# Kernel tuning notes

Measured on AMD Instinct MI355X. Metric: run time of the kernel, lower is better.

Reference implementation:

```python
import jax, jax.numpy as jnp
import numpy as np
from jax import lax

# dims: T timesteps, CIN=6 DoG channels, HxW image; F conv filters, K kernel
T, CIN, H, W_IN = 15, 6, 512, 512
F, K, PAD = 64, 5, 2
THRESH = 15.0
K_WTA, RADIUS = 5, 2  # self.k1, self.r1


def setup_inputs() -> dict:
    key = jax.random.key(0)
    k1, k2 = jax.random.split(key)
    # cumulative binary spike wave: once a unit spikes it stays 1 (SpykeTorch convention)
    ev = (jax.random.uniform(k1, (T, CIN, H, W_IN)) < 0.02).astype(jnp.float32)
    x = jnp.clip(jnp.cumsum(ev, axis=0), 0.0, 1.0)
    w = 0.8 + 0.05 * jax.random.normal(k2, (F, CIN, K, K), dtype=jnp.float32)
    return {"x": x, "w": w}


def _pool_pad(x, pad):
    # sf.pooling(x, 2, 2): max-pool 2x2 stride 2; sf.pad: zero pad
    x = lax.reduce_window(x, -jnp.inf, lax.max, (1, 1, 2, 2), (1, 1, 2, 2), 'VALID')
    return jnp.pad(x, ((0, 0), (0, 0), (pad, pad), (pad, pad)))


def _fire(pot, thr):
    # sf.fire(pot, thr, True): zero sub-threshold potentials, spikes = sign
    tp = jnp.where(pot < thr, 0.0, pot)
    return jnp.sign(tp), tp


def _pointwise_inhibition(pot):
    # keep, per spatial site, only the feature with the earliest (then strongest) spike
    T_ = pot.shape[0]
    max_vals = jnp.max(pot, axis=1, keepdims=True)      # [T,1,H,W]
    max_idx = jnp.argmax(pot, axis=1, keepdims=True)    # [T,1,H,W]
    clamp = jnp.sign(max_vals)                          # 1 where any feature active
    earliest = jnp.clip(T_ - jnp.sum(clamp, axis=0, keepdims=True), 0, T_ - 1).astype(jnp.int32)  # [1,1,H,W]
    winners = jnp.take_along_axis(max_idx, earliest, axis=0)  # [1,1,H,W] winning feature
    has_spike = clamp[-1:]                              # [1,1,H,W] any spike by last step
    ch = jnp.arange(pot.shape[1]).reshape(1, -1, 1, 1)
    coef = jnp.where(ch == winners, has_spike, 0.0)     # scatter of winner coeff
    return pot * coef


def _get_k_winners(pot, spikes, k, radius):
    # NMS-like radius-based k-winners-take-all over [F,H,W]
    T_ = pot.shape[0]
    earliest = jnp.clip(T_ - jnp.sum(spikes, axis=0, keepdims=True), 0, T_ - 1).astype(jnp.int32)
    values = jnp.take_along_axis(pot, earliest, axis=0)  # potential at earliest spike
    trunc = spikes * values
    v = jnp.max(trunc) * T_  # large bias favoring earlier spikes
    total = jnp.sum(trunc + spikes * v, axis=0)          # [F,H,W]
    Fc, Hh, Ww = total.shape
    feat = jnp.arange(Fc).reshape(-1, 1, 1)
    row = jnp.arange(Hh).reshape(1, -1, 1)
    col = jnp.arange(Ww).reshape(1, 1, -1)
    winners = []
    for _ in range(k):  # small fixed k (5), fine to unroll
        idx = jnp.argmax(total)
        val = jnp.reshape(total, (-1,))[idx]
        f, r, c = jnp.unravel_index(idx, total.shape)
        active = val != 0
        win = jnp.where(active, jnp.stack([f, r, c]).astype(jnp.int32),
                        jnp.full((3,), -1, jnp.int32))
        winners.append(win)
        suppress = (feat == f) | ((jnp.abs(row - r) <= radius) & (jnp.abs(col - c) <= radius))
        total = jnp.where(active & suppress, 0.0, total)
    return jnp.stack(winners)  # [k,3] with -1 rows when fewer winners exist


def reference(x, w):
    inp = _pool_pad(x, PAD)  # [T,6,260,260]
    pot = lax.conv_general_dilated(inp, w, (1, 1), 'VALID',
                                   dimension_numbers=('NCHW', 'OIHW', 'NCHW'))  # [T,F,256,256]
    spk, pot = _fire(pot, THRESH)
    pot = _pointwise_inhibition(pot)
    spk = jnp.sign(pot)
    winners = _get_k_winners(pot, spk, K_WTA, RADIUS)
    return spk, winners
```

## Files before the change

### kernel.cpp

```cpp
#include <hip/hip_runtime.h>
#include <hip/hip_bf16.h>

#define T_ 15
#define CIN_ 6
#define F_ 64
#define HW_ 256
#define PW_ 260
#define THRESH_ 15.0f
#define TAU_NEVER 15


__global__ __launch_bounds__(256) void pool_tau(const float* __restrict__ x,
                                                unsigned char* __restrict__ tau) {
    int idx = blockIdx.x * 256 + threadIdx.x;
    if (idx >= CIN_ * HW_ * HW_) return;
    int xx = idx & 255;
    int yy = (idx >> 8) & 255;
    int c  = idx >> 16;
    const float* base = x + ((size_t)c * 512 + 2 * yy) * 512 + 2 * xx;
    int tval = TAU_NEVER;
    for (int t = 0; t < T_; ++t) {
        float2 a = *(const float2*)(base);
        float2 b = *(const float2*)(base + 512);
        if (a.x > 0.f || a.y > 0.f || b.x > 0.f || b.y > 0.f) { tval = t; break; }
        base += (size_t)CIN_ * 512 * 512;
    }
    tau[(c * PW_ + (yy + 2)) * PW_ + (xx + 2)] = (unsigned char)tval;
}

__global__ __launch_bounds__(256, 2) void phaseA(const unsigned char* __restrict__ tau,
                                                 const float* __restrict__ w,
                                                 int* __restrict__ rec_wch,
                                                 float* __restrict__ rec_val,
                                                 int* __restrict__ rec_e,
                                                 unsigned int* __restrict__ gmaxp) {
    __shared__ float wl[F_ * 172];
    __shared__ unsigned char tw[CIN_ * 144];
    __shared__ float red[64 * 65];
    __shared__ float pm[64 * 5];
    __shared__ int   pa[64 * 5];
    __shared__ unsigned char donef[64];
    __shared__ int doneG[4];
    __shared__ int doneAll;
    __shared__ int bmaxBits;

    const int tid = threadIdx.x;
    const int f = tid & 63;
    const int g = tid >> 6;
    const int gx = (g & 1) * 4;
    const int gy = (g >> 1) * 4;
    const int px0 = blockIdx.x * 8;
    const int py0 = blockIdx.y * 8;

    if (tid < 64) donef[tid] = 0;
    if (tid < 4) doneG[tid] = 0;
    if (tid == 0) { doneAll = 0; bmaxBits = 0; }

    for (int idx = tid; idx < F_ * 150; idx += 256) {
        int ff = idx / 150, r = idx - ff * 150;
        int c = r / 25, k = r - c * 25;
        wl[ff * 172 + c * 28 + k] = w[idx];
    }
    for (int idx = tid; idx < CIN_ * 144; idx += 256) {
        int c = idx / 144;
        int rem = idx - c * 144;
        int r = rem / 12;
        int xx = rem - r * 12;
        tw[idx] = tau[(c * PW_ + (py0 + r)) * PW_ + (px0 + xx)];
    }
    __syncthreads();

    for (int t = 0; t < T_; ++t) {
        bool waveActive = (doneG[g] < 16);

        if (waveActive) {
            float acc[16];
#pragma unroll
            for (int i = 0; i < 16; ++i) acc[i] = 0.0f;

            for (int c = 0; c < CIN_; ++c) {
                float win[8][8];
                const unsigned char* tb = &tw[c * 144 + gy * 12 + gx];
#pragma unroll
                for (int r = 0; r < 8; ++r) {
                    unsigned int lo = *(const unsigned int*)(tb + r * 12);
                    unsigned int hi = *(const unsigned int*)(tb + r * 12 + 4);
#pragma unroll
                    for (int b = 0; b < 4; ++b) {
                        win[r][b]     = (((lo >> (8 * b)) & 0xFF) <= (unsigned)t) ? 1.0f : 0.0f;
                        win[r][4 + b] = (((hi >> (8 * b)) & 0xFF) <= (unsigned)t) ? 1.0f : 0.0f;
                    }
                }
                float wr[28];
#pragma unroll
                for (int q = 0; q < 7; ++q)
                    *(float4*)&wr[4 * q] = *(const float4*)&wl[f * 172 + c * 28 + 4 * q];
#pragma unroll
                for (int ki = 0; ki < 5; ++ki)
#pragma unroll
                    for (int kj = 0; kj < 5; ++kj) {
                        float wv = wr[ki * 5 + kj];
#pragma unroll
                        for (int py = 0; py < 4; ++py)
#pragma unroll
                            for (int px = 0; px < 4; ++px)
                                acc[py * 4 + px] += win[py + ki][px + kj] * wv;
                    }
            }
#pragma unroll
            for (int i = 0; i < 16; ++i) {
                float v = acc[i];
                v = (v < THRESH_) ? 0.0f : v;
                int py = i >> 2, px = i & 3;
                int pxl = (gy + py) * 8 + (gx + px);
                red[pxl * 65 + f] = v;
            }
        }
        __syncthreads();

        {
            int pxl = tid & 63, ch = tid >> 6;
            if (!donef[pxl]) {
                float m = -1.0f; int a = 0;
#pragma unroll
                for (int k = 0; k < 16; ++k) {
                    float v = red[pxl * 65 + ch * 16 + k];
                    if (v > m) { m = v; a = ch * 16 + k; }
                }
                pm[pxl * 5 + ch] = m;
                pa[pxl * 5 + ch] = a;
            }
        }
        __syncthreads();

        if (tid < 64 && !donef[tid]) {
            float m = pm[tid * 5]; int a = pa[tid * 5];
#pragma unroll
            for (int ch = 1; ch < 4; ++ch) {
                float v = pm[tid * 5 + ch];
                if (v > m) { m = v; a = pa[tid * 5 + ch]; }
            }
            if (m > 0.0f) {
                int gyg = py0 + (tid >> 3), gxg = px0 + (tid & 7);
                int p = gyg * HW_ + gxg;
                rec_wch[p] = a;
                rec_val[p] = m;
                rec_e[p] = t;
                donef[tid] = 1;
                int gyp = tid >> 3, gxp = tid & 7;
                int gOf = ((gyp >= 4) ? 2 : 0) + ((gxp >= 4) ? 1 : 0);
                atomicAdd(&doneG[gOf], 1);
                atomicAdd(&doneAll, 1);
                atomicMax(&bmaxBits, __float_as_int(m));
            }
        }
        __syncthreads();
        if (doneAll == 64) break;
    }

    if (tid < 64 && !donef[tid]) {
        int gyg = py0 + (tid >> 3), gxg = px0 + (tid & 7);
        int p = gyg * HW_ + gxg;
        rec_wch[p] = -1;
        rec_val[p] = 0.0f;
        rec_e[p] = T_;
    }
    if (tid == 0 && bmaxBits != 0)
        atomicMax(gmaxp, (unsigned int)bmaxBits);
}

__global__ __launch_bounds__(256) void render(const int* __restrict__ rec_wch,
                                              const int* __restrict__ rec_e,
                                              float* __restrict__ out) {
    const int tid = threadIdx.x;
    const int t = blockIdx.y;
    const int px = blockIdx.x * 1024 + tid * 4;

    int4 wch4 = *(const int4*)(rec_wch + px);
    int4 e4   = *(const int4*)(rec_e + px);
    int s0 = (wch4.x >= 0 && t >= e4.x) ? wch4.x : -1;
    int s1 = (wch4.y >= 0 && t >= e4.y) ? wch4.y : -1;
    int s2 = (wch4.z >= 0 && t >= e4.z) ? wch4.z : -1;
    int s3 = (wch4.w >= 0 && t >= e4.w) ? wch4.w : -1;

    float* base = out + (((size_t)t * F_) << 16) + px;
#pragma unroll
    for (int f = 0; f < F_; ++f) {
        float4 v;
        v.x = (f == s0) ? 1.0f : 0.0f;
        v.y = (f == s1) ? 1.0f : 0.0f;
        v.z = (f == s2) ? 1.0f : 0.0f;
        v.w = (f == s3) ? 1.0f : 0.0f;
        *(float4*)(base + ((size_t)f << 16)) = v;
    }
}

__global__ __launch_bounds__(256) void compute_total(const int* __restrict__ rec_wch,
                                                     const float* __restrict__ rec_val,
                                                     const int* __restrict__ rec_e,
                                                     const unsigned int* __restrict__ gmaxp,
                                                     float* __restrict__ total) {
    int i = blockIdx.x * 256 + threadIdx.x;
    int wch = rec_wch[i];
    float g = __uint_as_float(*gmaxp);
    float v15 = 15.0f * g;
    float tot = 0.0f;
    if (wch >= 0) {
        int e = rec_e[i];
        float base = rec_val[i] + v15;
        for (int t = e; t < T_; ++t) tot += base;
    }
    total[i] = tot;
}

__global__ __launch_bounds__(256) void max_round(const float* __restrict__ total,
                                                 const int* __restrict__ rec_wch,
                                                 unsigned long long* __restrict__ slots,
                                                 int round) {
    __shared__ unsigned long long sred[256];
    int i = blockIdx.x * 256 + threadIdx.x;
    float v = total[i];
    unsigned long long key = 0ULL;
    if (v > 0.0f) {
        int fch = rec_wch[i];
        int r = i >> 8, c = i & 255;
        bool sup = false;
        for (int j = 0; j < round; ++j) {
            unsigned long long s = slots[j];
            if (s == 0ULL) continue;
            int fl = 0x7fffffff - (int)(unsigned int)(s & 0xffffffffu);
            int fj = fl >> 16, rj = (fl >> 8) & 255, cj = fl & 255;
            int dr = r - rj; if (dr < 0) dr = -dr;
            int dc = c - cj; if (dc < 0) dc = -dc;
            if (fch == fj || (dr <= 2 && dc <= 2)) sup = true;
        }
        if (!sup) {
            int fl = (fch << 16) | i;
            unsigned int comp = 0x7fffffffu - (unsigned int)fl;
            key = ((unsigned long long)__float_as_uint(v) << 32) | comp;
        }
    }
    sred[threadIdx.x] = key;
    __syncthreads();
    for (int s = 128; s > 0; s >>= 1) {
        if (threadIdx.x < s) {
            if (sred[threadIdx.x + s] > sred[threadIdx.x]) sred[threadIdx.x] = sred[threadIdx.x + s];
        }
        __syncthreads();
    }
    if (threadIdx.x == 0 && sred[0] != 0ULL)
        atomicMax(&slots[round], sred[0]);
}

__global__ void writer(const unsigned long long* __restrict__ slots,
                       float* __restrict__ out) {
    int r = threadIdx.x;
    if (r < 5) {
        unsigned long long s = slots[r];
        float* wout = out + (size_t)T_ * F_ * HW_ * HW_ + r * 3;
        if (s != 0ULL) {
            int fl = 0x7fffffff - (int)(unsigned int)(s & 0xffffffffu);
            wout[0] = (float)(fl >> 16);
            wout[1] = (float)((fl >> 8) & 255);
            wout[2] = (float)(fl & 255);
        } else {
            wout[0] = -1.0f; wout[1] = -1.0f; wout[2] = -1.0f;
        }
    }
}

extern "C" void kernel_launch(void* const* d_in, const int* in_sizes, int n_in,
                              void* d_out, int out_size, void* d_ws, size_t ws_size,
                              hipStream_t stream) {
    const float* x = (const float*)d_in[0];
    const float* w = (const float*)d_in[1];
    float* out = (float*)d_out;

    char* wsc = (char*)d_ws;
    unsigned char* tau = (unsigned char*)wsc;
    size_t off = (size_t)CIN_ * PW_ * PW_;
    int* rec_wch = (int*)(wsc + off);        off += 65536 * sizeof(int);
    float* rec_val = (float*)(wsc + off);    off += 65536 * sizeof(float);
    int* rec_e = (int*)(wsc + off);          off += 65536 * sizeof(int);
    float* total = (float*)(wsc + off);      off += 65536 * sizeof(float);
    unsigned long long* slots = (unsigned long long*)(wsc + off);  off += 5 * sizeof(unsigned long long);
    unsigned int* gmaxp = (unsigned int*)(wsc + off);

    hipMemsetAsync(tau, 0x0F, (size_t)CIN_ * PW_ * PW_, stream);
    hipMemsetAsync(slots, 0, 5 * sizeof(unsigned long long) + sizeof(unsigned int), stream);

    pool_tau<<<(CIN_ * HW_ * HW_ + 255) / 256, 256, 0, stream>>>(x, tau);
    phaseA<<<dim3(32, 32), 256, 0, stream>>>(tau, w, rec_wch, rec_val, rec_e, gmaxp);
    render<<<dim3(64, 15), 256, 0, stream>>>(rec_wch, rec_e, out);
    compute_total<<<256, 256, 0, stream>>>(rec_wch, rec_val, rec_e, gmaxp, total);
    for (int r = 0; r < 5; ++r)
        max_round<<<256, 256, 0, stream>>>(total, rec_wch, slots, r);
    writer<<<1, 64, 0, stream>>>(slots, out);
}
```

Measured before the change: 483.7 us.

## Replace shared-memory channel argmax with wave shuffles and binary-search first-spike time

New measurement: 471.3 us. 1.03x faster.

```diff
diff --git a/kernel.cpp b/kernel.cpp
--- a/kernel.cpp
+++ b/kernel.cpp
@@ -11,55 +11,64 @@
 
 
 __global__ __launch_bounds__(256) void pool_tau(const float* __restrict__ x,
-                                                unsigned char* __restrict__ tau) {
+                                                unsigned char* __restrict__ tau,
+                                                unsigned long long* __restrict__ slots,
+                                                unsigned int* __restrict__ gmaxp) {
     int idx = blockIdx.x * 256 + threadIdx.x;
-    if (idx >= CIN_ * HW_ * HW_) return;
-    int xx = idx & 255;
-    int yy = (idx >> 8) & 255;
-    int c  = idx >> 16;
-    const float* base = x + ((size_t)c * 512 + 2 * yy) * 512 + 2 * xx;
-    int tval = TAU_NEVER;
-    for (int t = 0; t < T_; ++t) {
-        float2 a = *(const float2*)(base);
-        float2 b = *(const float2*)(base + 512);
-        if (a.x > 0.f || a.y > 0.f || b.x > 0.f || b.y > 0.f) { tval = t; break; }
-        base += (size_t)CIN_ * 512 * 512;
-    }
-    tau[(c * PW_ + (yy + 2)) * PW_ + (xx + 2)] = (unsigned char)tval;
-}
-
-__global__ __launch_bounds__(256, 2) void phaseA(const unsigned char* __restrict__ tau,
+    if (idx < 5) slots[idx] = 0ULL;
+    if (idx == 5) *gmaxp = 0u;
+    if (idx >= CIN_ * PW_ * PW_) return;
+    int xx = idx % PW_;
+    int rest = idx / PW_;
+    int yy = rest % PW_;
+    int c = rest / PW_;
+    unsigned char tv = TAU_NEVER;
+    if (xx >= 2 && xx < 258 && yy >= 2 && yy < 258) {
+        int i = yy - 2, j = xx - 2;
+        const float* b0 = x + ((size_t)c * 512 + 2 * i) * 512 + 2 * j;
+        const size_t tstride = (size_t)CIN_ * 512 * 512;
+        {
+            const float* b = b0 + 14 * tstride;
+            float2 a = *(const float2*)b;
+            float2 d = *(const float2*)(b + 512);
+            if (a.x > 0.f || a.y > 0.f || d.x > 0.f || d.y > 0.f) {
+                int lo = 0, hi = 14;
+                while (lo < hi) {
+                    int mid = (lo + hi) >> 1;
+                    const float* bm = b0 + (size_t)mid * tstride;
+                    float2 am = *(const float2*)bm;
+                    float2 dm = *(const float2*)(bm + 512);
+                    bool on = (am.x > 0.f || am.y > 0.f || dm.x > 0.f || dm.y > 0.f);
+                    if (on) hi = mid; else lo = mid + 1;
+                }
+                tv = (unsigned char)lo;
+            }
+        }
+    }
+    tau[idx] = tv;
+}
+
+__global__ __launch_bounds__(256, 3) void phaseA(const unsigned char* __restrict__ tau,
                                                  const float* __restrict__ w,
                                                  int* __restrict__ rec_wch,
                                                  float* __restrict__ rec_val,
                                                  int* __restrict__ rec_e,
                                                  unsigned int* __restrict__ gmaxp) {
-    __shared__ float wl[F_ * 172];
+    __shared__ float wl2[150 * 64];
     __shared__ unsigned char tw[CIN_ * 144];
-    __shared__ float red[64 * 65];
-    __shared__ float pm[64 * 5];
-    __shared__ int   pa[64 * 5];
-    __shared__ unsigned char donef[64];
-    __shared__ int doneG[4];
-    __shared__ int doneAll;
-    __shared__ int bmaxBits;
+    __shared__ float wmax[4];
 
     const int tid = threadIdx.x;
-    const int f = tid & 63;
+    const int lane = tid & 63;
     const int g = tid >> 6;
     const int gx = (g & 1) * 4;
     const int gy = (g >> 1) * 4;
     const int px0 = blockIdx.x * 8;
     const int py0 = blockIdx.y * 8;
 
-    if (tid < 64) donef[tid] = 0;
-    if (tid < 4) doneG[tid] = 0;
-    if (tid == 0) { doneAll = 0; bmaxBits = 0; }
-
-    for (int idx = tid; idx < F_ * 150; idx += 256) {
-        int ff = idx / 150, r = idx - ff * 150;
-        int c = r / 25, k = r - c * 25;
-        wl[ff * 172 + c * 28 + k] = w[idx];
+    for (int idx = tid; idx < 9600; idx += 256) {
+        int k = idx >> 6, f = idx & 63;
+        wl2[idx] = w[f * 150 + k];
     }
     for (int idx = tid; idx < CIN_ * 144; idx += 256) {
         int c = idx / 144;
@@ -70,103 +79,78 @@
     }
     __syncthreads();
 
+    unsigned int done = 0;
+    int myw = -1, mye = T_;
+    float myv = 0.0f;
+    float wavemax = 0.0f;
+
     for (int t = 0; t < T_; ++t) {
-        bool waveActive = (doneG[g] < 16);
-
-        if (waveActive) {
-            float acc[16];
-#pragma unroll
-            for (int i = 0; i < 16; ++i) acc[i] = 0.0f;
-
-            for (int c = 0; c < CIN_; ++c) {
-                float win[8][8];
-                const unsigned char* tb = &tw[c * 144 + gy * 12 + gx];
-#pragma unroll
-                for (int r = 0; r < 8; ++r) {
-                    unsigned int lo = *(const unsigned int*)(tb + r * 12);
-                    unsigned int hi = *(const unsigned int*)(tb + r * 12 + 4);
-#pragma unroll
-                    for (int b = 0; b < 4; ++b) {
-                        win[r][b]     = (((lo >> (8 * b)) & 0xFF) <= (unsigned)t) ? 1.0f : 0.0f;
-                        win[r][4 + b] = (((hi >> (8 * b)) & 0xFF) <= (unsigned)t) ? 1.0f : 0.0f;
-                    }
-                }
-                float wr[28];
-#pragma unroll
-                for (int q = 0; q < 7; ++q)
-                    *(float4*)&wr[4 * q] = *(const float4*)&wl[f * 172 + c * 28 + 4 * q];
-#pragma unroll
-                for (int ki = 0; ki < 5; ++ki)
-#pragma unroll
-                    for (int kj = 0; kj < 5; ++kj) {
-                        float wv = wr[ki * 5 + kj];
-#pragma unroll
-                        for (int py = 0; py < 4; ++py)
-#pragma unroll
-                            for (int px = 0; px < 4; ++px)
-                                acc[py * 4 + px] += win[py + ki][px + kj] * wv;
-                    }
+        float acc[16];
+#pragma unroll
+        for (int i = 0; i < 16; ++i) acc[i] = 0.0f;
+
+        for (int c = 0; c < CIN_; ++c) {
+            float win[8][8];
+            const unsigned char* tb = &tw[c * 144 + gy * 12 + gx];
+#pragma unroll
+            for (int r = 0; r < 8; ++r) {
+                unsigned int lo = *(const unsigned int*)(tb + r * 12);
+                unsigned int hi = *(const unsigned int*)(tb + r * 12 + 4);
+#pragma unroll
+                for (int b = 0; b < 4; ++b) {
+                    win[r][b]     = (((lo >> (8 * b)) & 0xFF) <= (unsigned)t) ? 1.0f : 0.0f;
+                    win[r][4 + b] = (((hi >> (8 * b)) & 0xFF) <= (unsigned)t) ? 1.0f : 0.0f;
+                }
             }
 #pragma unroll
-            for (int i = 0; i < 16; ++i) {
-                float v = acc[i];
-                v = (v < THRESH_) ? 0.0f : v;
-                int py = i >> 2, px = i & 3;
-                int pxl = (gy + py) * 8 + (gx + px);
-                red[pxl * 65 + f] = v;
+            for (int ki = 0; ki < 5; ++ki)
+#pragma unroll
+                for (int kj = 0; kj < 5; ++kj) {
+                    float wv = wl2[((c * 25 + ki * 5 + kj) << 6) + lane];
+#pragma unroll
+                    for (int py = 0; py < 4; ++py)
+#pragma unroll
+                        for (int px = 0; px < 4; ++px)
+                            acc[py * 4 + px] += win[py + ki][px + kj] * wv;
+                }
+        }
+
+#pragma unroll
+        for (int i = 0; i < 16; ++i) {
+            if (done & (1u << i)) continue;
+            float v = acc[i];
+            v = (v < THRESH_) ? 0.0f : v;
+            if (__any(v > 0.0f)) {
+                unsigned long long key =
+                    ((unsigned long long)__float_as_uint(v) << 6) | (unsigned)(63 - lane);
+#pragma unroll
+                for (int m = 1; m < 64; m <<= 1) {
+                    unsigned long long o = __shfl_xor(key, m, 64);
+                    if (o > key) key = o;
+                }
+                float mv = __uint_as_float((unsigned int)(key >> 6));
+                int wf = 63 - (int)(key & 63ULL);
+                done |= (1u << i);
+                if (lane == i) { myw = wf; myv = mv; mye = t; }
+                wavemax = fmaxf(wavemax, mv);
             }
         }
-        __syncthreads();
-
-        {
-            int pxl = tid & 63, ch = tid >> 6;
-            if (!donef[pxl]) {
-                float m = -1.0f; int a = 0;
-#pragma unroll
-                for (int k = 0; k < 16; ++k) {
-                    float v = red[pxl * 65 + ch * 16 + k];
-                    if (v > m) { m = v; a = ch * 16 + k; }
-                }
-                pm[pxl * 5 + ch] = m;
-                pa[pxl * 5 + ch] = a;
-            }
-        }
-        __syncthreads();
-
-        if (tid < 64 && !donef[tid]) {
-            float m = pm[tid * 5]; int a = pa[tid * 5];
-#pragma unroll
-            for (int ch = 1; ch < 4; ++ch) {
-                float v = pm[tid * 5 + ch];
-                if (v > m) { m = v; a = pa[tid * 5 + ch]; }
-            }
-            if (m > 0.0f) {
-                int gyg = py0 + (tid >> 3), gxg = px0 + (tid & 7);
-                int p = gyg * HW_ + gxg;
-                rec_wch[p] = a;
-                rec_val[p] = m;
-                rec_e[p] = t;
-                donef[tid] = 1;
-                int gyp = tid >> 3, gxp = tid & 7;
-                int gOf = ((gyp >= 4) ? 2 : 0) + ((gxp >= 4) ? 1 : 0);
-                atomicAdd(&doneG[gOf], 1);
-                atomicAdd(&doneAll, 1);
-                atomicMax(&bmaxBits, __float_as_int(m));
-            }
-        }
-        __syncthreads();
-        if (doneAll == 64) break;
-    }
-
-    if (tid < 64 && !donef[tid]) {
-        int gyg = py0 + (tid >> 3), gxg = px0 + (tid & 7);
-        int p = gyg * HW_ + gxg;
-        rec_wch[p] = -1;
-        rec_val[p] = 0.0f;
-        rec_e[p] = T_;
-    }
-    if (tid == 0 && bmaxBits != 0)
-        atomicMax(gmaxp, (unsigned int)bmaxBits);
+        if (done == 0xFFFFu) break;
+    }
+
+    if (lane < 16) {
+        int py = lane >> 2, px = lane & 3;
+        int p = (py0 + gy + py) * HW_ + (px0 + gx + px);
+        rec_wch[p] = myw;
+        rec_val[p] = myv;
+        rec_e[p] = mye;
+    }
+    if (lane == 0) wmax[g] = wavemax;
+    __syncthreads();
+    if (tid == 0) {
+        float m = fmaxf(fmaxf(wmax[0], wmax[1]), fmaxf(wmax[2], wmax[3]));
+        if (m > 0.0f) atomicMax(gmaxp, __float_as_uint(m));
+    }
 }
 
 __global__ __launch_bounds__(256) void render(const int* __restrict__ rec_wch,
@@ -286,10 +270,7 @@
     unsigned long long* slots = (unsigned long long*)(wsc + off);  off += 5 * sizeof(unsigned long long);
     unsigned int* gmaxp = (unsigned int*)(wsc + off);
 
-    hipMemsetAsync(tau, 0x0F, (size_t)CIN_ * PW_ * PW_, stream);
-    hipMemsetAsync(slots, 0, 5 * sizeof(unsigned long long) + sizeof(unsigned int), stream);
-
-    pool_tau<<<(CIN_ * HW_ * HW_ + 255) / 256, 256, 0, stream>>>(x, tau);
+    pool_tau<<<(CIN_ * PW_ * PW_ + 255) / 256, 256, 0, stream>>>(x, tau, slots, gmaxp);
     phaseA<<<dim3(32, 32), 256, 0, stream>>>(tau, w, rec_wch, rec_val, rec_e, gmaxp);
     render<<<dim3(64, 15), 256, 0, stream>>>(rec_wch, rec_e, out);
     compute_total<<<256, 256, 0, stream>>>(rec_wch, rec_val, rec_e, gmaxp, total);
```
